# Kernel optimization log

Measured on AMD Instinct MI355X. Metric: run time of the kernel, lower is better.

Reference implementation:

```python
import jax, jax.numpy as jnp
import numpy as np

N = 100000
E = 1600000
IN_CH = 128
HID = 128
OUT_CH = 1
EPS = 1e-5


def setup_inputs() -> dict:
    key = jax.random.key(0)
    ks = jax.random.split(key, 20)
    x = jax.random.normal(ks[0], (N, IN_CH), dtype=jnp.float32)
    edge_index = jax.random.randint(ks[1], (2, E), 0, N, dtype=jnp.int64)

    def lin(k, fi, fo):
        k1, k2 = jax.random.split(k)
        s = 1.0 / np.sqrt(fi)
        W = jax.random.uniform(k1, (fi, fo), jnp.float32, -s, s)
        b = jax.random.uniform(k2, (fo,), jnp.float32, -s, s)
        return W, b

    W1, b1 = lin(ks[2], IN_CH, HID)
    W2, b2 = lin(ks[3], HID, HID)
    Wf1, bf1 = lin(ks[4], HID, HID)
    Wf2, bf2 = lin(ks[5], HID, HID)
    Wo, bo = lin(ks[6], HID, OUT_CH)

    def bn(k):
        k1, k2, k3, k4 = jax.random.split(k, 4)
        gamma = 1.0 + 0.1 * jax.random.normal(k1, (HID,), jnp.float32)
        beta = 0.1 * jax.random.normal(k2, (HID,), jnp.float32)
        mean = 0.1 * jax.random.normal(k3, (HID,), jnp.float32)
        var = 0.5 + jax.random.uniform(k4, (HID,), jnp.float32)
        return gamma, beta, mean, var

    g1, be1, m1, v1 = bn(ks[7])
    g2, be2, m2, v2 = bn(ks[8])
    g3, be3, m3, v3 = bn(ks[9])

    return dict(x=x, edge_index=edge_index,
                W1=W1, b1=b1, W2=W2, b2=b2,
                Wf1=Wf1, bf1=bf1, Wf2=Wf2, bf2=bf2, Wo=Wo, bo=bo,
                g1=g1, be1=be1, m1=m1, v1=v1,
                g2=g2, be2=be2, m2=m2, v2=v2,
                g3=g3, be3=be3, m3=m3, v3=v3)


def _gcn_conv(x, W, b, src, dst):
    # PyG GCNConv: add self-loops, symmetric normalization deg^-1/2 A deg^-1/2.
    loop = jnp.arange(N, dtype=src.dtype)
    s = jnp.concatenate([src, loop])   # [E+N]
    d = jnp.concatenate([dst, loop])   # [E+N]
    deg = jax.ops.segment_sum(jnp.ones(s.shape[0], x.dtype), d, num_segments=N)
    dinv = jnp.where(deg > 0, jax.lax.rsqrt(deg), 0.0)
    h = x @ W                          # [N, out]
    norm = (dinv[s] * dinv[d])[:, None]  # [E+N, 1]
    msg = h[s] * norm                  # gather + scale, [E+N, out]
    out = jax.ops.segment_sum(msg, d, num_segments=N)  # scatter-add
    return out + b


def _bn(x, gamma, beta, mean, var):
    # BatchNorm1d in inference mode (dropout treated as eval/identity).
    return (x - mean) * jax.lax.rsqrt(var + EPS) * gamma + beta


def reference(x, edge_index, W1, b1, W2, b2, Wf1, bf1, Wf2, bf2, Wo, bo,
              g1, be1, m1, v1, g2, be2, m2, v2, g3, be3, m3, v3):
    src, dst = edge_index[0], edge_index[1]
    h = jax.nn.relu(_bn(_gcn_conv(x, W1, b1, src, dst), g1, be1, m1, v1))
    h = jax.nn.relu(_bn(_gcn_conv(h, W2, b2, src, dst), g2, be2, m2, v2))
    h = jax.nn.relu(_bn(h @ Wf1 + bf1, g3, be3, m3, v3))
    h1 = jax.nn.relu(h @ Wf2 + bf2)
    raw_pred = jax.nn.softplus(h1 @ Wo + bo).reshape(-1)
    return (raw_pred, h1)
```

## Files before the change

kernel.cpp:

```cpp
#include <hip/hip_runtime.h>
#include <math.h>

#define EPS_BN 1e-5f
#define MAXNB 512

typedef __attribute__((ext_vector_type(8))) short bf16x8;
typedef __attribute__((ext_vector_type(4))) float f32x4;
typedef __attribute__((ext_vector_type(2))) float f32x2;

__device__ __forceinline__ ushort f2bf(float f) {
    uint u = __float_as_uint(f);
    u += 0x7FFF + ((u >> 16) & 1);
    return (ushort)(u >> 16);
}
__device__ __forceinline__ float bf2f(uint h) {
    return __uint_as_float(h << 16);
}
__device__ __forceinline__ unsigned char f2fp8(float v) {
    uint q = __builtin_amdgcn_cvt_pk_fp8_f32(v, v, 0, false);
    return (unsigned char)(q & 0xff);
}

__global__ __launch_bounds__(256) void prep_k(const float* __restrict__ W1,
                                              const float* __restrict__ W2,
                                              const float* __restrict__ W3,
                                              const float* __restrict__ W4,
                                              ushort* __restrict__ T1,
                                              ushort* __restrict__ T2,
                                              ushort* __restrict__ T3,
                                              ushort* __restrict__ T4,
                                              int* __restrict__ bcur, int NB, int stride,
                                              const float* __restrict__ b1,
                                              const float* __restrict__ g1,
                                              const float* __restrict__ be1,
                                              const float* __restrict__ m1,
                                              const float* __restrict__ v1,
                                              const float* __restrict__ b2,
                                              const float* __restrict__ g2,
                                              const float* __restrict__ be2,
                                              const float* __restrict__ m2,
                                              const float* __restrict__ v2,
                                              float* __restrict__ bnc) {
    if (blockIdx.x == 256) {
        for (int i = threadIdx.x; i < NB; i += 256) bcur[i] = i * stride;
        int cc = threadIdx.x & 127;
        int l2 = threadIdx.x >> 7;
        const float* gg = l2 ? g2 : g1;
        const float* bb = l2 ? be2 : be1;
        const float* mm = l2 ? m2 : m1;
        const float* vv = l2 ? v2 : v1;
        const float* bi = l2 ? b2 : b1;
        float s = gg[cc] * rsqrtf(vv[cc] + EPS_BN);
        float* o = bnc + l2 * 256;
        o[cc] = s;
        o[128 + cc] = bb[cc] + (bi[cc] - mm[cc]) * s;
        return;
    }
    int which = blockIdx.x >> 6;
    const float* W = (which == 0) ? W1 : (which == 1) ? W2 : (which == 2) ? W3 : W4;
    ushort* T = (which == 0) ? T1 : (which == 1) ? T2 : (which == 2) ? T3 : T4;
    int i = (blockIdx.x & 63) * 256 + threadIdx.x;
    int n = i >> 7, k = i & 127;
    T[n * 128 + k] = f2bf(W[k * 128 + n]);
}

__global__ __launch_bounds__(256) void bucketA_k(const int* __restrict__ src,
                                                 const int* __restrict__ dst,
                                                 int* __restrict__ bcur,
                                                 int* __restrict__ coarse, int nE, int NB) {
    __shared__ int cnt[MAXNB];
    __shared__ int basix[MAXNB];
    const int tid = threadIdx.x;
    for (int i = tid; i < NB; i += 256) cnt[i] = 0;
    __syncthreads();
    int base = blockIdx.x * 4096;
    int es[16], ed[16], rk[16];
#pragma unroll
    for (int i = 0; i < 16; i++) {
        int e = base + i * 256 + tid;
        if (e < nE) {
            es[i] = src[e];
            ed[i] = dst[e];
            rk[i] = atomicAdd(&cnt[ed[i] >> 8], 1);
        } else {
            ed[i] = -1;
        }
    }
    __syncthreads();
    for (int i = tid; i < NB; i += 256)
        if (cnt[i]) basix[i] = atomicAdd(&bcur[i], cnt[i]);
    __syncthreads();
#pragma unroll
    for (int i = 0; i < 16; i++) {
        if (ed[i] >= 0)
            coarse[basix[ed[i] >> 8] + rk[i]] = es[i] | ((ed[i] & 255) << 24);
    }
}

__global__ __launch_bounds__(256) void bucketB_k(const int* __restrict__ coarse,
                                                 const int* __restrict__ bcur,
                                                 int2* __restrict__ rowptr,
                                                 int* __restrict__ col,
                                                 float* __restrict__ dinv, int N,
                                                 int stride) {
    __shared__ int cnt[256];
    __shared__ int s[256];
    __shared__ int cur[256];
    const int tid = threadIdx.x;
    const int b = blockIdx.x;
    const int beg = b * stride, end = bcur[b];
    cnt[tid] = 0;
    __syncthreads();
    for (int p = beg + tid; p < end; p += 256)
        atomicAdd(&cnt[((uint)coarse[p]) >> 24], 1);
    __syncthreads();
    int c = cnt[tid];
    s[tid] = c;
    __syncthreads();
    for (int off = 1; off < 256; off <<= 1) {
        int v = (tid >= off) ? s[tid - off] : 0;
        __syncthreads();
        s[tid] += v;
        __syncthreads();
    }
    int ex = s[tid] - c;
    int node = b * 256 + tid;
    if (node < N) {
        rowptr[node] = make_int2(beg + ex, beg + ex + c);
        dinv[node] = rsqrtf((float)c + 1.0f);
    }
    cur[tid] = ex;
    __syncthreads();
    for (int p = beg + tid; p < end; p += 256) {
        int v = coarse[p];
        int r = atomicAdd(&cur[((uint)v) >> 24], 1);
        col[beg + r] = v & 0xFFFFFF;
    }
}

__device__ __forceinline__ void add8p(f32x2* acc, uint2 a) {
    acc[0] += __builtin_amdgcn_cvt_pk_f32_fp8(a.x, false);
    acc[1] += __builtin_amdgcn_cvt_pk_f32_fp8(a.x, true);
    acc[2] += __builtin_amdgcn_cvt_pk_f32_fp8(a.y, false);
    acc[3] += __builtin_amdgcn_cvt_pk_f32_fp8(a.y, true);
}

__global__ __launch_bounds__(256) void gather_k(const unsigned char* __restrict__ h8,
                                                const int2* __restrict__ rowptr,
                                                const int* __restrict__ col,
                                                const float* __restrict__ dinv,
                                                const float* __restrict__ sc,
                                                const float* __restrict__ sh,
                                                ushort* __restrict__ out, int n) {
    int node = blockIdx.x * 4 + (threadIdx.x >> 6);
    if (node >= n) return;
    int lane = threadIdx.x & 63;
    int grp = lane >> 4;
    int li = lane & 15;
    const uint c = (uint)(li * 8);
    const uint c2 = c + (uint)(grp * 2);

    int2 rp = rowptr[node];
    float dd = dinv[node];
    f32x2 s2 = *(const f32x2*)(sc + c2);
    f32x2 h2 = *(const f32x2*)(sh + c2);

    int beg = rp.x, end = rp.y;
    int deg = end - beg;
    int nfull = deg >> 4;

    f32x2 acc[4];
#pragma unroll
    for (int j = 0; j < 4; j++) acc[j] = (f32x2){0.f, 0.f};

    if (grp == 0) {
        uint2 rv = *(const uint2*)(h8 + (((uint)node << 7) | c));
        add8p(acc, rv);
    }

    int pt = beg + grp + (nfull << 4);
    bool v0 = pt < end, v1 = pt + 4 < end, v2 = pt + 8 < end, v3 = pt + 12 < end;
    int t0 = v0 ? __builtin_nontemporal_load(col + pt) : node;
    int t1 = v1 ? __builtin_nontemporal_load(col + pt + 4) : node;
    int t2 = v2 ? __builtin_nontemporal_load(col + pt + 8) : node;
    int t3 = v3 ? __builtin_nontemporal_load(col + pt + 12) : node;

    int p = beg + grp;
    for (int it = 0; it < nfull; ++it, p += 16) {
        int s0 = __builtin_nontemporal_load(col + p);
        int s1 = __builtin_nontemporal_load(col + p + 4);
        int s2i = __builtin_nontemporal_load(col + p + 8);
        int s3 = __builtin_nontemporal_load(col + p + 12);
        uint2 a0 = *(const uint2*)(h8 + (((uint)s0 << 7) | c));
        uint2 a1 = *(const uint2*)(h8 + (((uint)s1 << 7) | c));
        uint2 a2 = *(const uint2*)(h8 + (((uint)s2i << 7) | c));
        uint2 a3 = *(const uint2*)(h8 + (((uint)s3 << 7) | c));
        add8p(acc, a0);
        add8p(acc, a1);
        add8p(acc, a2);
        add8p(acc, a3);
    }
    {
        uint2 a0 = *(const uint2*)(h8 + (((uint)t0 << 7) | c));
        uint2 a1 = *(const uint2*)(h8 + (((uint)t1 << 7) | c));
        uint2 a2 = *(const uint2*)(h8 + (((uint)t2 << 7) | c));
        uint2 a3 = *(const uint2*)(h8 + (((uint)t3 << 7) | c));
        if (!v0) { a0.x = 0u; a0.y = 0u; }
        if (!v1) { a1.x = 0u; a1.y = 0u; }
        if (!v2) { a2.x = 0u; a2.y = 0u; }
        if (!v3) { a3.x = 0u; a3.y = 0u; }
        add8p(acc, a0);
        add8p(acc, a1);
        add8p(acc, a2);
        add8p(acc, a3);
    }
#pragma unroll
    for (int j = 0; j < 4; j++) {
        f32x2 t;
        t.x = __shfl_xor(acc[j].x, 16, 64);
        t.y = __shfl_xor(acc[j].y, 16, 64);
        acc[j] += t;
        t.x = __shfl_xor(acc[j].x, 32, 64);
        t.y = __shfl_xor(acc[j].y, 32, 64);
        acc[j] += t;
    }
    f32x2 pr = (grp == 0) ? acc[0] : (grp == 1) ? acc[1] : (grp == 2) ? acc[2] : acc[3];
    float o0 = fmaxf(fmaf(pr.x * dd, s2.x, h2.x), 0.0f);
    float o1 = fmaxf(fmaf(pr.y * dd, s2.y, h2.y), 0.0f);
    uint r = (uint)f2bf(o0) | ((uint)f2bf(o1) << 16);
    *(uint*)&out[(size_t)node * 128 + c2] = r;
}

template <int MODE, int F32IN>
__global__ __launch_bounds__(256) void mfma_gemm_k(const void* __restrict__ Xin,
                                                   const ushort* __restrict__ Wt,
                                                   const float* __restrict__ dinvp,
                                                   const float* __restrict__ bias,
                                                   const float* __restrict__ g,
                                                   const float* __restrict__ be,
                                                   const float* __restrict__ mn,
                                                   const float* __restrict__ vr,
                                                   const float* __restrict__ Wo,
                                                   const float* __restrict__ bo,
                                                   float* __restrict__ pred,
                                                   void* __restrict__ Y, int nrows) {
    constexpr int LDK = 136;
    __shared__ ushort sX[64 * LDK];
    __shared__ ushort sW[128 * LDK];
    __shared__ float red[64];
    __shared__ float sD[64];
    const int tid = threadIdx.x;
    const int row0 = blockIdx.x * 64;

#pragma unroll
    for (int i = 0; i < 8; i++) {
        int c = tid + i * 256;
        int r = c >> 4, o = c & 15;
        *(int4*)&sW[r * LDK + o * 8] = *(const int4*)&Wt[r * 128 + o * 8];
    }
    if (F32IN) {
        const float* Xf = (const float*)Xin;
#pragma unroll
        for (int i = 0; i < 8; i++) {
            int c = tid + i * 256;
            int r = c >> 5, o = c & 31;
            int rg = row0 + r;
            if (rg >= nrows) rg = nrows - 1;
            float4 v = *(const float4*)&Xf[(size_t)rg * 128 + o * 4];
            ushort4 u = {f2bf(v.x), f2bf(v.y), f2bf(v.z), f2bf(v.w)};
            *(ushort4*)&sX[r * LDK + o * 4] = u;
        }
    } else {
        const ushort* Xb = (const ushort*)Xin;
#pragma unroll
        for (int i = 0; i < 4; i++) {
            int c = tid + i * 256;
            int r = c >> 4, o = c & 15;
            int rg = row0 + r;
            if (rg >= nrows) rg = nrows - 1;
            *(int4*)&sX[r * LDK + o * 8] = *(const int4*)&Xb[(size_t)rg * 128 + o * 8];
        }
    }
    if (MODE == 2 && tid < 64) red[tid] = 0.0f;
    if (MODE == 0 && tid < 64) {
        int rg = row0 + tid;
        sD[tid] = dinvp[(rg < nrows) ? rg : (nrows - 1)];
    }
    __syncthreads();

    const int wave = tid >> 6, lane = tid & 63;
    const int rw = (wave >> 1) * 32;
    const int cw = (wave & 1) * 64;
    const int lm = lane & 15, lq = lane >> 4;

    f32x4 acc[2][4];
#pragma unroll
    for (int tr = 0; tr < 2; tr++)
#pragma unroll
        for (int tc = 0; tc < 4; tc++) acc[tr][tc] = (f32x4){0.f, 0.f, 0.f, 0.f};

#pragma unroll
    for (int ks = 0; ks < 4; ks++) {
        int kb = ks * 32 + lq * 8;
        bf16x8 a[2], b[4];
#pragma unroll
        for (int tr = 0; tr < 2; tr++)
            a[tr] = *(bf16x8*)&sX[(rw + tr * 16 + lm) * LDK + kb];
#pragma unroll
        for (int tc = 0; tc < 4; tc++)
            b[tc] = *(bf16x8*)&sW[(cw + tc * 16 + lm) * LDK + kb];
#pragma unroll
        for (int tr = 0; tr < 2; tr++)
#pragma unroll
            for (int tc = 0; tc < 4; tc++)
                acc[tr][tc] = __builtin_amdgcn_mfma_f32_16x16x32_bf16(a[tr], b[tc],
                                                                      acc[tr][tc], 0, 0, 0);
    }

    float part[8];
    if (MODE == 2) {
#pragma unroll
        for (int i = 0; i < 8; i++) part[i] = 0.0f;
    }
#pragma unroll
    for (int tc = 0; tc < 4; tc++) {
        int c = cw + tc * 16 + lm;
        float psc, psh;
        if (MODE == 1) {
            float sc = g[c] * rsqrtf(vr[c] + EPS_BN);
            psc = sc;
            psh = be[c] + (bias[c] - mn[c]) * sc;
        } else if (MODE == 2) {
            psc = 1.0f;
            psh = bias[c];
        } else {
            psc = 1.0f;
            psh = 0.0f;
        }
        float woc = (MODE == 2) ? Wo[c] : 0.0f;
#pragma unroll
        for (int tr = 0; tr < 2; tr++) {
#pragma unroll
            for (int r = 0; r < 4; r++) {
                int lrow = rw + tr * 16 + lq * 4 + r;
                int row = row0 + lrow;
                if (row < nrows) {
                    float v = acc[tr][tc][r];
                    if (MODE == 0) {
                        ((unsigned char*)Y)[(size_t)row * 128 + c] = f2fp8(v * sD[lrow]);
                    } else if (MODE == 1) {
                        v = fmaxf(v * psc + psh, 0.0f);
                        ((ushort*)Y)[(size_t)row * 128 + c] = f2bf(v);
                    } else {
                        v = fmaxf(v + psh, 0.0f);
                        ((float*)Y)[(size_t)row * 128 + c] = v;
                        part[tr * 4 + r] = fmaf(v, woc, part[tr * 4 + r]);
                    }
                }
            }
        }
    }
    if (MODE == 2) {
#pragma unroll
        for (int tr = 0; tr < 2; tr++)
#pragma unroll
            for (int r = 0; r < 4; r++)
                atomicAdd(&red[rw + tr * 16 + lq * 4 + r], part[tr * 4 + r]);
        __syncthreads();
        if (tid < 64) {
            int row = row0 + tid;
            if (row < nrows) {
                float xv = red[tid] + bo[0];
                pred[row] = fmaxf(xv, 0.0f) + log1pf(expf(-fabsf(xv)));
            }
        }
    }
}

extern "C" void kernel_launch(void* const* d_in, const int* in_sizes, int n_in,
                              void* d_out, int out_size, void* d_ws, size_t ws_size,
                              hipStream_t stream) {
    const float* x = (const float*)d_in[0];
    const int* ei = (const int*)d_in[1];
    const int N = in_sizes[0] / 128;
    const int E = in_sizes[1] / 2;
    const int* srcv = ei;
    const int* dstv = ei + E;
    const float* W1 = (const float*)d_in[2];  const float* b1 = (const float*)d_in[3];
    const float* W2 = (const float*)d_in[4];  const float* b2 = (const float*)d_in[5];
    const float* Wf1 = (const float*)d_in[6]; const float* bf1 = (const float*)d_in[7];
    const float* Wf2 = (const float*)d_in[8]; const float* bf2 = (const float*)d_in[9];
    const float* Wo = (const float*)d_in[10]; const float* bo = (const float*)d_in[11];
    const float* g1 = (const float*)d_in[12], *be1 = (const float*)d_in[13],
               *m1 = (const float*)d_in[14], *v1 = (const float*)d_in[15];
    const float* g2 = (const float*)d_in[16], *be2 = (const float*)d_in[17],
               *m2 = (const float*)d_in[18], *v2 = (const float*)d_in[19];
    const float* g3 = (const float*)d_in[20], *be3 = (const float*)d_in[21],
               *m3 = (const float*)d_in[22], *v3 = (const float*)d_in[23];

    char* ws = (char*)d_ws;
    size_t off = 0;
    auto carve = [&](size_t bytes) {
        char* p = ws + off;
        off = (off + bytes + 255) & ~(size_t)255;
        return p;
    };
    const int NB = (N + 255) >> 8;
    const int STRIDE = ((E / NB + 511) + 255) & ~255;
    int* bcur = (int*)carve((size_t)MAXNB * 4);
    int2* rowptr = (int2*)carve((size_t)N * 8);
    int* col = (int*)carve((size_t)NB * STRIDE * 4);
    int* coarse = (int*)carve((size_t)NB * STRIDE * 4);
    float* dinv = (float*)carve((size_t)N * 4);
    unsigned char* bufA8 = (unsigned char*)carve((size_t)N * 128);
    ushort* bufB = (ushort*)carve((size_t)N * 128 * 2);
    ushort* bufC = (ushort*)carve((size_t)N * 128 * 2);
    ushort* Wt1 = (ushort*)carve(128 * 128 * 2);
    ushort* Wt2 = (ushort*)carve(128 * 128 * 2);
    ushort* Wtf1 = (ushort*)carve(128 * 128 * 2);
    ushort* Wtf2 = (ushort*)carve(128 * 128 * 2);
    float* bnc = (float*)carve(512 * 4);

    float* out_pred = (float*)d_out;
    float* out_h1 = out_pred + N;

    const int gblocks = (N + 63) / 64;
    const int tblocks = (E + 4095) / 4096;
    const int wblocks = (N + 3) / 4;

    prep_k<<<257, 256, 0, stream>>>(W1, W2, Wf1, Wf2, Wt1, Wt2, Wtf1, Wtf2, bcur, NB,
                                    STRIDE, b1, g1, be1, m1, v1, b2, g2, be2, m2, v2,
                                    bnc);
    bucketA_k<<<tblocks, 256, 0, stream>>>(srcv, dstv, bcur, coarse, E, NB);
    bucketB_k<<<NB, 256, 0, stream>>>(coarse, bcur, rowptr, col, dinv, N, STRIDE);

    mfma_gemm_k<0, 1><<<gblocks, 256, 0, stream>>>(x, Wt1, dinv, nullptr, nullptr,
                                                   nullptr, nullptr, nullptr, nullptr,
                                                   nullptr, nullptr, bufA8, N);
    gather_k<<<wblocks, 256, 0, stream>>>(bufA8, rowptr, col, dinv,
                                          bnc, bnc + 128, bufB, N);
    mfma_gemm_k<0, 0><<<gblocks, 256, 0, stream>>>(bufB, Wt2, dinv, nullptr, nullptr,
                                                   nullptr, nullptr, nullptr, nullptr,
                                                   nullptr, nullptr, bufA8, N);
    gather_k<<<wblocks, 256, 0, stream>>>(bufA8, rowptr, col, dinv,
                                          bnc + 256, bnc + 384, bufB, N);
    mfma_gemm_k<1, 0><<<gblocks, 256, 0, stream>>>(bufB, Wtf1, nullptr, bf1, g3, be3, m3,
                                                   v3, nullptr, nullptr, nullptr, bufC, N);
    mfma_gemm_k<2, 0><<<gblocks, 256, 0, stream>>>(bufC, Wtf2, nullptr, bf2, nullptr,
                                                   nullptr, nullptr, nullptr, Wo, bo,
                                                   out_pred, out_h1, N);
}
```

Measured before the change: 346.3 us.

## Permute weight columns so GEMM epilogue stores four contiguous outputs per lane

```diff
diff --git a/kernel.cpp b/kernel.cpp
--- a/kernel.cpp
+++ b/kernel.cpp
@@ -15,10 +15,6 @@
 }
 __device__ __forceinline__ float bf2f(uint h) {
     return __uint_as_float(h << 16);
-}
-__device__ __forceinline__ unsigned char f2fp8(float v) {
-    uint q = __builtin_amdgcn_cvt_pk_fp8_f32(v, v, 0, false);
-    return (unsigned char)(q & 0xff);
 }
 
 __global__ __launch_bounds__(256) void prep_k(const float* __restrict__ W1,
@@ -40,20 +36,32 @@
                                               const float* __restrict__ be2,
                                               const float* __restrict__ m2,
                                               const float* __restrict__ v2,
+                                              const float* __restrict__ b3,
+                                              const float* __restrict__ g3,
+                                              const float* __restrict__ be3,
+                                              const float* __restrict__ m3,
+                                              const float* __restrict__ v3,
                                               float* __restrict__ bnc) {
     if (blockIdx.x == 256) {
         for (int i = threadIdx.x; i < NB; i += 256) bcur[i] = i * stride;
         int cc = threadIdx.x & 127;
         int l2 = threadIdx.x >> 7;
-        const float* gg = l2 ? g2 : g1;
-        const float* bb = l2 ? be2 : be1;
-        const float* mm = l2 ? m2 : m1;
-        const float* vv = l2 ? v2 : v1;
-        const float* bi = l2 ? b2 : b1;
-        float s = gg[cc] * rsqrtf(vv[cc] + EPS_BN);
-        float* o = bnc + l2 * 256;
-        o[cc] = s;
-        o[128 + cc] = bb[cc] + (bi[cc] - mm[cc]) * s;
+        {
+            const float* gg = l2 ? g2 : g1;
+            const float* bb = l2 ? be2 : be1;
+            const float* mm = l2 ? m2 : m1;
+            const float* vv = l2 ? v2 : v1;
+            const float* bi = l2 ? b2 : b1;
+            float s = gg[cc] * rsqrtf(vv[cc] + EPS_BN);
+            float* o = bnc + l2 * 256;
+            o[cc] = s;
+            o[128 + cc] = bb[cc] + (bi[cc] - mm[cc]) * s;
+        }
+        if (threadIdx.x < 128) {
+            float s = g3[cc] * rsqrtf(v3[cc] + EPS_BN);
+            bnc[512 + cc] = s;
+            bnc[640 + cc] = be3[cc] + (b3[cc] - m3[cc]) * s;
+        }
         return;
     }
     int which = blockIdx.x >> 6;
@@ -61,7 +69,9 @@
     ushort* T = (which == 0) ? T1 : (which == 1) ? T2 : (which == 2) ? T3 : T4;
     int i = (blockIdx.x & 63) * 256 + threadIdx.x;
     int n = i >> 7, k = i & 127;
-    T[n * 128 + k] = f2bf(W[k * 128 + n]);
+    int idx = n & 63;
+    int nperm = (n & 64) | ((idx & 3) << 4) | (idx >> 2);
+    T[nperm * 128 + k] = f2bf(W[k * 128 + n]);
 }
 
 __global__ __launch_bounds__(256) void bucketA_k(const int* __restrict__ src,
@@ -236,10 +246,8 @@
                                                    const ushort* __restrict__ Wt,
                                                    const float* __restrict__ dinvp,
                                                    const float* __restrict__ bias,
-                                                   const float* __restrict__ g,
-                                                   const float* __restrict__ be,
-                                                   const float* __restrict__ mn,
-                                                   const float* __restrict__ vr,
+                                                   const float* __restrict__ scp,
+                                                   const float* __restrict__ shp,
                                                    const float* __restrict__ Wo,
                                                    const float* __restrict__ bo,
                                                    float* __restrict__ pred,
@@ -317,46 +325,58 @@
                                                                       acc[tr][tc], 0, 0, 0);
     }
 
+    const int c0 = cw + (lm << 2);
+    float psc[4], psh[4], woc[4];
+#pragma unroll
+    for (int tc = 0; tc < 4; tc++) {
+        int c = c0 + tc;
+        if (MODE == 1) {
+            psc[tc] = scp[c];
+            psh[tc] = shp[c];
+        } else if (MODE == 2) {
+            psh[tc] = bias[c];
+            woc[tc] = Wo[c];
+        }
+    }
     float part[8];
     if (MODE == 2) {
 #pragma unroll
         for (int i = 0; i < 8; i++) part[i] = 0.0f;
     }
 #pragma unroll
-    for (int tc = 0; tc < 4; tc++) {
-        int c = cw + tc * 16 + lm;
-        float psc, psh;
-        if (MODE == 1) {
-            float sc = g[c] * rsqrtf(vr[c] + EPS_BN);
-            psc = sc;
-            psh = be[c] + (bias[c] - mn[c]) * sc;
-        } else if (MODE == 2) {
-            psc = 1.0f;
-            psh = bias[c];
-        } else {
-            psc = 1.0f;
-            psh = 0.0f;
-        }
-        float woc = (MODE == 2) ? Wo[c] : 0.0f;
-#pragma unroll
-        for (int tr = 0; tr < 2; tr++) {
-#pragma unroll
-            for (int r = 0; r < 4; r++) {
-                int lrow = rw + tr * 16 + lq * 4 + r;
-                int row = row0 + lrow;
-                if (row < nrows) {
-                    float v = acc[tr][tc][r];
-                    if (MODE == 0) {
-                        ((unsigned char*)Y)[(size_t)row * 128 + c] = f2fp8(v * sD[lrow]);
-                    } else if (MODE == 1) {
-                        v = fmaxf(v * psc + psh, 0.0f);
-                        ((ushort*)Y)[(size_t)row * 128 + c] = f2bf(v);
-                    } else {
-                        v = fmaxf(v + psh, 0.0f);
-                        ((float*)Y)[(size_t)row * 128 + c] = v;
-                        part[tr * 4 + r] = fmaf(v, woc, part[tr * 4 + r]);
-                    }
-                }
+    for (int tr = 0; tr < 2; tr++) {
+#pragma unroll
+        for (int r = 0; r < 4; r++) {
+            int lrow = rw + tr * 16 + lq * 4 + r;
+            int row = row0 + lrow;
+            if (row >= nrows) continue;
+            if (MODE == 0) {
+                float dd = sD[lrow];
+                uint q = __builtin_amdgcn_cvt_pk_fp8_f32(acc[tr][0][r] * dd,
+                                                         acc[tr][1][r] * dd, 0u, false);
+                q = __builtin_amdgcn_cvt_pk_fp8_f32(acc[tr][2][r] * dd,
+                                                    acc[tr][3][r] * dd, q, true);
+                *(uint*)((unsigned char*)Y + (size_t)row * 128 + c0) = q;
+            } else if (MODE == 1) {
+                float o0 = fmaxf(fmaf(acc[tr][0][r], psc[0], psh[0]), 0.0f);
+                float o1 = fmaxf(fmaf(acc[tr][1][r], psc[1], psh[1]), 0.0f);
+                float o2 = fmaxf(fmaf(acc[tr][2][r], psc[2], psh[2]), 0.0f);
+                float o3 = fmaxf(fmaf(acc[tr][3][r], psc[3], psh[3]), 0.0f);
+                uint2 st;
+                st.x = (uint)f2bf(o0) | ((uint)f2bf(o1) << 16);
+                st.y = (uint)f2bf(o2) | ((uint)f2bf(o3) << 16);
+                *(uint2*)((ushort*)Y + (size_t)row * 128 + c0) = st;
+            } else {
+                float o0 = fmaxf(acc[tr][0][r] + psh[0], 0.0f);
+                float o1 = fmaxf(acc[tr][1][r] + psh[1], 0.0f);
+                float o2 = fmaxf(acc[tr][2][r] + psh[2], 0.0f);
+                float o3 = fmaxf(acc[tr][3][r] + psh[3], 0.0f);
+                float4 st = {o0, o1, o2, o3};
+                *(float4*)((float*)Y + (size_t)row * 128 + c0) = st;
+                part[tr * 4 + r] = fmaf(o0, woc[0],
+                                   fmaf(o1, woc[1],
+                                   fmaf(o2, woc[2],
+                                   fmaf(o3, woc[3], part[tr * 4 + r]))));
             }
         }
     }
@@ -419,7 +439,7 @@
     ushort* Wt2 = (ushort*)carve(128 * 128 * 2);
     ushort* Wtf1 = (ushort*)carve(128 * 128 * 2);
     ushort* Wtf2 = (ushort*)carve(128 * 128 * 2);
-    float* bnc = (float*)carve(512 * 4);
+    float* bnc = (float*)carve(768 * 4);
 
     float* out_pred = (float*)d_out;
     float* out_h1 = out_pred + N;
@@ -430,23 +450,24 @@
 
     prep_k<<<257, 256, 0, stream>>>(W1, W2, Wf1, Wf2, Wt1, Wt2, Wtf1, Wtf2, bcur, NB,
                                     STRIDE, b1, g1, be1, m1, v1, b2, g2, be2, m2, v2,
-                                    bnc);
+                                    bf1, g3, be3, m3, v3, bnc);
     bucketA_k<<<tblocks, 256, 0, stream>>>(srcv, dstv, bcur, coarse, E, NB);
     bucketB_k<<<NB, 256, 0, stream>>>(coarse, bcur, rowptr, col, dinv, N, STRIDE);
 
     mfma_gemm_k<0, 1><<<gblocks, 256, 0, stream>>>(x, Wt1, dinv, nullptr, nullptr,
                                                    nullptr, nullptr, nullptr, nullptr,
-                                                   nullptr, nullptr, bufA8, N);
+                                                   bufA8, N);
     gather_k<<<wblocks, 256, 0, stream>>>(bufA8, rowptr, col, dinv,
                                           bnc, bnc + 128, bufB, N);
     mfma_gemm_k<0, 0><<<gblocks, 256, 0, stream>>>(bufB, Wt2, dinv, nullptr, nullptr,
                                                    nullptr, nullptr, nullptr, nullptr,
-                                                   nullptr, nullptr, bufA8, N);
+                                                   bufA8, N);
     gather_k<<<wblocks, 256, 0, stream>>>(bufA8, rowptr, col, dinv,
                                           bnc + 256, bnc + 384, bufB, N);
-    mfma_gemm_k<1, 0><<<gblocks, 256, 0, stream>>>(bufB, Wtf1, nullptr, bf1, g3, be3, m3,
-                                                   v3, nullptr, nullptr, nullptr, bufC, N);
+    mfma_gemm_k<1, 0><<<gblocks, 256, 0, stream>>>(bufB, Wtf1, nullptr, nullptr,
+                                                   bnc + 512, bnc + 640, nullptr,
+                                                   nullptr, nullptr, bufC, N);
     mfma_gemm_k<2, 0><<<gblocks, 256, 0, stream>>>(bufC, Wtf2, nullptr, bf2, nullptr,
-                                                   nullptr, nullptr, nullptr, Wo, bo,
+                                                   nullptr, Wo, bo,
                                                    out_pred, out_h1, N);
 }
```

Result: faster. 337.4 us (-2.6%).
